# Optimization experiments

Measured on AMD Instinct MI355X. Metric: run time of the kernel, lower is better.

## Reference

```python
import jax, jax.numpy as jnp
import numpy as np

N_DRUG = 20000
N_DIS = 40000
E = 500000
D_IN = 128
D_OUT = 128
SLOPE = 0.01  # F.leaky_relu default negative_slope


def setup_inputs() -> dict:
    key = jax.random.key(0)
    ks = jax.random.split(key, 17)
    s = 1.0 / np.sqrt(D_IN)
    inp = {
        'feat_drug': jax.random.normal(ks[0], (N_DRUG, D_IN), jnp.float32),
        'feat_disease': jax.random.normal(ks[1], (N_DIS, D_IN), jnp.float32),
        'src_ind': jax.random.randint(ks[2], (E,), 0, N_DRUG, jnp.int32),
        'dst_ind': jax.random.randint(ks[3], (E,), 0, N_DIS, jnp.int32),
        'src_rev': jax.random.randint(ks[4], (E,), 0, N_DIS, jnp.int32),
        'dst_rev': jax.random.randint(ks[5], (E,), 0, N_DRUG, jnp.int32),
        'src_dd': jax.random.randint(ks[6], (E,), 0, N_DIS, jnp.int32),
        'dst_dd': jax.random.randint(ks[7], (E,), 0, N_DIS, jnp.int32),
        'W_ind': jax.random.normal(ks[8], (D_IN, D_OUT), jnp.float32) * s,
        'b_ind': jax.random.normal(ks[9], (D_OUT,), jnp.float32) * s,
        'W_rev': jax.random.normal(ks[10], (D_IN, D_OUT), jnp.float32) * s,
        'b_rev': jax.random.normal(ks[11], (D_OUT,), jnp.float32) * s,
        'W_dd': jax.random.normal(ks[12], (D_IN, D_OUT), jnp.float32) * s,
        'b_dd': jax.random.normal(ks[13], (D_OUT,), jnp.float32) * s,
        'a_ind': jax.random.normal(ks[14], (2 * D_OUT,), jnp.float32) * s,
        'a_rev': jax.random.normal(ks[15], (2 * D_OUT,), jnp.float32) * s,
        'a_dd': jax.random.normal(ks[16], (2 * D_OUT,), jnp.float32) * s,
    }
    return inp


def _leaky(x):
    return jnp.where(x >= 0, x, SLOPE * x)


def _etype_softmax_agg(wh_src, wh_dst, src, dst, a, n_dst):
    # per-edge message gather
    m = wh_src[src]                      # [E, D_OUT]
    wd = wh_dst[dst]                     # [E, D_OUT]
    # attn_fc(concat(m, wd)) == m @ a[:D] + wd @ a[D:]
    e = _leaky(m @ a[:D_OUT] + wd @ a[D_OUT:])   # [E]
    # segment softmax over dst (per-node mailbox softmax)
    emax = jax.ops.segment_max(e, dst, num_segments=n_dst)
    ex = jnp.exp(e - emax[dst])
    denom = jax.ops.segment_sum(ex, dst, num_segments=n_dst)
    alpha = ex / denom[dst]
    # weighted scatter-sum aggregation
    return jax.ops.segment_sum(alpha[:, None] * m, dst, num_segments=n_dst)


def reference(feat_drug, feat_disease, src_ind, dst_ind, src_rev, dst_rev,
              src_dd, dst_dd, W_ind, b_ind, W_rev, b_rev, W_dd, b_dd,
              a_ind, a_rev, a_dd):
    # per-etype linear projections of the source node type
    Wh_ind = feat_drug @ W_ind + b_ind       # drug nodes, etype 'indication'
    Wh_rev = feat_disease @ W_rev + b_rev    # disease nodes, etype 'rev_indication'
    Wh_dd = feat_disease @ W_dd + b_dd       # disease nodes, etype 'dd' (self type)
    # indication: drug->disease pairs with dst key Wh_rev_indication
    h_dis = _etype_softmax_agg(Wh_ind, Wh_rev, src_ind, dst_ind, a_ind, N_DIS)
    # dd: same src/dst type, uses Wh_dd on both sides; cross-etype 'sum' reducer
    h_dis = h_dis + _etype_softmax_agg(Wh_dd, Wh_dd, src_dd, dst_dd, a_dd, N_DIS)
    # rev_indication: disease->drug pairs with dst key Wh_indication
    h_drug = _etype_softmax_agg(Wh_rev, Wh_ind, src_rev, dst_rev, a_rev, N_DRUG)
    return (h_drug, h_dis)
```

## Files before the change

### kernel.cpp

```cpp
#include <hip/hip_runtime.h>
#include <hip/hip_bf16.h>

#define N_DRUG 20000
#define N_DIS  40000
#define NE     500000
#define D      128
#define PITCH  136
#define NTOT   100000
#define NQ     (NE / 4)
#define NQ3    (3 * NQ)
#define CSTR   16
#define WSZ    (128 * PITCH)

typedef __hip_bfloat16 bf16;
typedef __attribute__((ext_vector_type(8))) short short8;
typedef __attribute__((ext_vector_type(4))) float floatx4;
typedef __attribute__((ext_vector_type(4))) unsigned short ushortx4;

__device__ __forceinline__ float b2f(bf16 x) { return __bfloat162float(x); }

#define GB_DRUG 313
#define GB_DIS  625
#define GB_ALL  (GB_DRUG + 2 * GB_DIS)
#define GH      ((NQ3 + 255) / 256)

__global__ void k_prep(const float* __restrict__ W_ind, const float* __restrict__ W_rev,
                       const float* __restrict__ W_dd, bf16* __restrict__ WbfT)
{
    const int et = blockIdx.x >> 4;
    const int sl = blockIdx.x & 15;
    const float* W = (et == 0) ? W_ind : (et == 1) ? W_rev : W_dd;
    bf16* out = WbfT + (size_t)et * WSZ;
    int idx = sl * 1024 + threadIdx.x;
#pragma unroll
    for (int r = 0; r < 4; ++r, idx += 256) {
        int k = idx >> 7, n = idx & 127;
        out[n * PITCH + k] = __float2bfloat16(W[idx]);
    }
}

__global__ void k_gh(const float* __restrict__ feat_drug, const float* __restrict__ feat_dis,
                     const bf16* __restrict__ WbfT,
                     const float* __restrict__ b_ind, const float* __restrict__ b_rev,
                     const float* __restrict__ b_dd,
                     const float* __restrict__ a_ind, const float* __restrict__ a_rev,
                     const float* __restrict__ a_dd,
                     bf16* __restrict__ Wh_ind, bf16* __restrict__ Wh_rev,
                     bf16* __restrict__ Wh_dd,
                     float* __restrict__ s_src_ind, float* __restrict__ s_dst_rev,
                     float* __restrict__ s_src_rev, float* __restrict__ s_dst_ind,
                     float* __restrict__ s_src_dd,  float* __restrict__ s_dst_dd,
                     const int4* __restrict__ d_ind, const int4* __restrict__ d_dd,
                     const int4* __restrict__ d_rev, int* __restrict__ cnt,
                     unsigned short* __restrict__ rank)
{
    __shared__ __align__(16) bf16 WT[128 * PITCH];
    __shared__ __align__(16) bf16 FS[64 * PITCH];
    const int tid = threadIdx.x;
    const int blk = blockIdx.x;

    int gemm_blk;
    if (blk < 2 * GH) {
        if (blk & 1) {
            const int i = (blk >> 1) * 256 + tid;
            if (i >= NQ3) return;
            int4 d; int boff;
            if (i < NQ)          { d = d_ind[i];          boff = 0; }
            else if (i < 2 * NQ) { d = d_dd[i - NQ];      boff = 40000; }
            else                 { d = d_rev[i - 2 * NQ]; boff = 80000; }
            ushortx4 r;
            r[0] = (unsigned short)atomicAdd(&cnt[(boff + d.x) * CSTR], 1);
            r[1] = (unsigned short)atomicAdd(&cnt[(boff + d.y) * CSTR], 1);
            r[2] = (unsigned short)atomicAdd(&cnt[(boff + d.z) * CSTR], 1);
            r[3] = (unsigned short)atomicAdd(&cnt[(boff + d.w) * CSTR], 1);
            *(ushortx4*)(rank + 4 * (size_t)i) = r;
            return;
        }
        gemm_blk = blk >> 1;
    } else {
        gemm_blk = GH + (blk - 2 * GH);
    }

    const float *feat, *bias, *a1, *a2;
    const bf16* Wt;
    bf16* Wh; float *s1, *s2;
    int M, row0;
    if (gemm_blk < GB_DRUG) {
        feat = feat_drug; M = N_DRUG; row0 = gemm_blk * 64;
        Wt = WbfT; bias = b_ind; a1 = a_ind; a2 = a_rev + D;
        Wh = Wh_ind; s1 = s_src_ind; s2 = s_dst_rev;
    } else if (gemm_blk < GB_DRUG + GB_DIS) {
        feat = feat_dis; M = N_DIS; row0 = (gemm_blk - GB_DRUG) * 64;
        Wt = WbfT + WSZ; bias = b_rev; a1 = a_rev; a2 = a_ind + D;
        Wh = Wh_rev; s1 = s_src_rev; s2 = s_dst_ind;
    } else {
        feat = feat_dis; M = N_DIS; row0 = (gemm_blk - GB_DRUG - GB_DIS) * 64;
        Wt = WbfT + 2 * WSZ; bias = b_dd; a1 = a_dd; a2 = a_dd + D;
        Wh = Wh_dd; s1 = s_src_dd; s2 = s_dst_dd;
    }

#pragma unroll
    for (int rep = 0; rep < 9; ++rep) {
        int off = rep * 2048 + tid * 8;
        if (off < WSZ)
            *(short8*)(WT + off) = *(const short8*)(Wt + off);
    }
#pragma unroll
    for (int rep = 0; rep < 8; ++rep) {
        int idx = rep * 1024 + tid * 4;
        int r = idx >> 7, k = idx & 127;
        int gr = row0 + r;
        float4 f4 = (gr < M) ? *(const float4*)(feat + (size_t)gr * D + k)
                             : make_float4(0.f, 0.f, 0.f, 0.f);
        FS[r * PITCH + k + 0] = __float2bfloat16(f4.x);
        FS[r * PITCH + k + 1] = __float2bfloat16(f4.y);
        FS[r * PITCH + k + 2] = __float2bfloat16(f4.z);
        FS[r * PITCH + k + 3] = __float2bfloat16(f4.w);
    }
    __syncthreads();

    const int wave = tid >> 6;
    const int lane = tid & 63;
    const int m0   = wave * 16;
    const int arow = lane & 15;
    const int kq   = lane >> 4;

    floatx4 acc[8];
#pragma unroll
    for (int t = 0; t < 8; ++t) acc[t] = (floatx4){0.f, 0.f, 0.f, 0.f};

#pragma unroll
    for (int ks = 0; ks < 4; ++ks) {
        const int kb = ks * 32 + kq * 8;
        short8 afrag = *(const short8*)(FS + (m0 + arow) * PITCH + kb);
#pragma unroll
        for (int t = 0; t < 8; ++t) {
            short8 bfrag = *(const short8*)(WT + (t * 16 + arow) * PITCH + kb);
            acc[t] = __builtin_amdgcn_mfma_f32_16x16x32_bf16(afrag, bfrag, acc[t], 0, 0, 0);
        }
    }

    const int crow = m0 + kq * 4;
    float p1[4] = {0.f, 0.f, 0.f, 0.f};
    float p2[4] = {0.f, 0.f, 0.f, 0.f};
#pragma unroll
    for (int t = 0; t < 8; ++t) {
        const int n = t * 16 + arow;
        const float bn = bias[n], a1n = a1[n], a2n = a2[n];
#pragma unroll
        for (int r = 0; r < 4; ++r) {
            float v = acc[t][r] + bn;
            int gr = row0 + crow + r;
            if (gr < M) Wh[(size_t)gr * D + n] = __float2bfloat16(v);
            p1[r] += v * a1n;
            p2[r] += v * a2n;
        }
    }
#pragma unroll
    for (int r = 0; r < 4; ++r) {
#pragma unroll
        for (int off = 1; off < 16; off <<= 1) {
            p1[r] += __shfl_xor(p1[r], off);
            p2[r] += __shfl_xor(p2[r], off);
        }
    }
    if (arow == 0) {
#pragma unroll
        for (int r = 0; r < 4; ++r) {
            int gr = row0 + crow + r;
            if (gr < M) { s1[gr] = p1[r]; s2[gr] = p2[r]; }
        }
    }
}

__global__ void k_base(const int* __restrict__ cnt, int* __restrict__ base,
                       int* __restrict__ cntp, int* __restrict__ total, int n)
{
    __shared__ int sd[256];
    __shared__ int sbase;
    const int tid = threadIdx.x;
    const int gid = blockIdx.x * 256 + tid;
    int c = (gid < n) ? cnt[gid * CSTR] : 0;
    sd[tid] = c;
    __syncthreads();
    for (int off = 1; off < 256; off <<= 1) {
        int v = (tid >= off) ? sd[tid - off] : 0;
        __syncthreads();
        sd[tid] += v;
        __syncthreads();
    }
    if (tid == 255) sbase = atomicAdd(total, sd[255]);
    __syncthreads();
    if (gid < n) {
        base[gid] = sbase + sd[tid] - c;
        cntp[gid] = c;
    }
}

__global__ void k_fill_rank(const int4* __restrict__ s_ind, const int4* __restrict__ d_ind,
                            const int4* __restrict__ s_dd,  const int4* __restrict__ d_dd,
                            const int4* __restrict__ s_rev, const int4* __restrict__ d_rev,
                            const int* __restrict__ base, const unsigned short* __restrict__ rank,
                            unsigned short* __restrict__ col)
{
    const int i = blockIdx.x * 256 + threadIdx.x;
    if (i >= NQ3) return;
    int4 d, s; int boff;
    if (i < NQ)          { d = d_ind[i];              s = s_ind[i];          boff = 0; }
    else if (i < 2 * NQ) { int j = i - NQ;     d = d_dd[j];  s = s_dd[j];  boff = 40000; }
    else                 { int j = i - 2 * NQ; d = d_rev[j]; s = s_rev[j]; boff = 80000; }
    ushortx4 r = *(const ushortx4*)(rank + 4 * (size_t)i);
    col[base[boff + d.x] + r[0]] = (unsigned short)s.x;
    col[base[boff + d.y] + r[1]] = (unsigned short)s.y;
    col[base[boff + d.z] + r[2]] = (unsigned short)s.z;
    col[base[boff + d.w] + r[3]] = (unsigned short)s.w;
}

__device__ __forceinline__ float2 agg_seg(int b, int c, const unsigned short* __restrict__ col,
                                          const float* __restrict__ ssrc, float sdv,
                                          const bf16* __restrict__ Whs, int lane)
{
    float ax = 0.f, ay = 0.f, dpart = 0.f;
    for (int t0 = 0; t0 < c; t0 += 64) {
        const int rem = c - t0;
        const int k = rem < 64 ? rem : 64;
        int myc = 0; float myex = 0.f;
        if (lane < k) {
            myc = col[b + t0 + lane];
            float e = ssrc[myc] + sdv;
            e = (e >= 0.f) ? e : 0.01f * e;
            myex = __expf(fminf(e, 30.f));
        }
        dpart += myex;
        const int kk = (k + 7) & ~7;
        for (int j = 0; j < kk; j += 8) {
            int sv[8]; float ev[8]; __hip_bfloat162 w[8];
#pragma unroll
            for (int u = 0; u < 8; ++u) {
                sv[u] = __shfl(myc, j + u);
                ev[u] = __shfl(myex, j + u);
            }
#pragma unroll
            for (int u = 0; u < 8; ++u)
                w[u] = *(const __hip_bfloat162*)(Whs + (size_t)sv[u] * D + 2 * lane);
#pragma unroll
            for (int u = 0; u < 8; ++u) {
                ax += ev[u] * b2f(w[u].x);
                ay += ev[u] * b2f(w[u].y);
            }
        }
    }
    float denom = dpart;
#pragma unroll
    for (int off = 32; off; off >>= 1) denom += __shfl_xor(denom, off);
    const float inv = (c > 0) ? 1.f / denom : 0.f;
    return make_float2(ax * inv, ay * inv);
}

__global__ void k_agg(const int* __restrict__ base, const int* __restrict__ cnt,
                      const unsigned short* __restrict__ col,
                      const float* __restrict__ ss_ind, const float* __restrict__ sd_ind,
                      const bf16* __restrict__ Wh_ind,
                      const float* __restrict__ ss_dd, const float* __restrict__ sd_dd,
                      const bf16* __restrict__ Wh_dd,
                      const float* __restrict__ ss_rev, const float* __restrict__ sd_rev,
                      const bf16* __restrict__ Wh_rev,
                      float* __restrict__ out_dis, float* __restrict__ out_drug)
{
    const int g    = (int)((blockIdx.x * blockDim.x + threadIdx.x) >> 6);
    const int lane = threadIdx.x & 63;
    if (g < N_DIS) {
        float2 r1 = agg_seg(base[g], cnt[g], col, ss_ind, sd_ind[g], Wh_ind, lane);
        float2 r2 = agg_seg(base[40000 + g], cnt[40000 + g], col, ss_dd, sd_dd[g], Wh_dd, lane);
        *(float2*)(out_dis + (size_t)g * D + 2 * lane) = make_float2(r1.x + r2.x, r1.y + r2.y);
    } else if (g < N_DIS + N_DRUG) {
        const int gg = g - N_DIS;
        float2 r = agg_seg(base[80000 + gg], cnt[80000 + gg], col, ss_rev, sd_rev[gg], Wh_rev, lane);
        *(float2*)(out_drug + (size_t)gg * D + 2 * lane) = r;
    }
}

extern "C" void kernel_launch(void* const* d_in, const int* in_sizes, int n_in,
                              void* d_out, int out_size, void* d_ws, size_t ws_size,
                              hipStream_t stream)
{
    const float* feat_drug = (const float*)d_in[0];
    const float* feat_dis  = (const float*)d_in[1];
    const int*   src_ind   = (const int*)d_in[2];
    const int*   dst_ind   = (const int*)d_in[3];
    const int*   src_rev   = (const int*)d_in[4];
    const int*   dst_rev   = (const int*)d_in[5];
    const int*   src_dd    = (const int*)d_in[6];
    const int*   dst_dd    = (const int*)d_in[7];
    const float* W_ind     = (const float*)d_in[8];
    const float* b_ind     = (const float*)d_in[9];
    const float* W_rev     = (const float*)d_in[10];
    const float* b_rev     = (const float*)d_in[11];
    const float* W_dd      = (const float*)d_in[12];
    const float* b_dd      = (const float*)d_in[13];
    const float* a_ind     = (const float*)d_in[14];
    const float* a_rev     = (const float*)d_in[15];
    const float* a_dd      = (const float*)d_in[16];

    float* out_drug = (float*)d_out;
    float* out_dis  = (float*)d_out + (size_t)N_DRUG * D;

    char* ws = (char*)d_ws;
    size_t off = 0;
    auto alloc = [&](size_t bytes) -> void* {
        void* p = ws + off;
        off += (bytes + 255) & ~(size_t)255;
        return p;
    };

    bf16* Wh_ind = (bf16*)alloc(sizeof(bf16) * (size_t)N_DRUG * D);
    bf16* Wh_rev = (bf16*)alloc(sizeof(bf16) * (size_t)N_DIS * D);
    bf16* Wh_dd  = (bf16*)alloc(sizeof(bf16) * (size_t)N_DIS * D);
    bf16* WbfT   = (bf16*)alloc(sizeof(bf16) * 3 * WSZ);

    float* s_src_ind = (float*)alloc(sizeof(float) * N_DRUG);
    float* s_dst_rev = (float*)alloc(sizeof(float) * N_DRUG);
    float* s_src_rev = (float*)alloc(sizeof(float) * N_DIS);
    float* s_dst_ind = (float*)alloc(sizeof(float) * N_DIS);
    float* s_src_dd  = (float*)alloc(sizeof(float) * N_DIS);
    float* s_dst_dd  = (float*)alloc(sizeof(float) * N_DIS);

    unsigned short* col  = (unsigned short*)alloc(sizeof(unsigned short) * 3 * NE);
    unsigned short* rank = (unsigned short*)alloc(sizeof(unsigned short) * 3 * NE);
    int* base = (int*)alloc(sizeof(int) * NTOT);
    int* cntp = (int*)alloc(sizeof(int) * NTOT);

    const size_t nzero = (size_t)NTOT * CSTR + 4;
    int* zr  = (int*)alloc(sizeof(int) * nzero);
    int* cnt = zr;
    int* total = zr + (size_t)NTOT * CSTR;

    hipMemsetAsync(zr, 0, sizeof(int) * nzero, stream);

    k_prep<<<48, 256, 0, stream>>>(W_ind, W_rev, W_dd, WbfT);

    k_gh<<<GB_ALL + GH, 256, 0, stream>>>(
        feat_drug, feat_dis, WbfT, b_ind, b_rev, b_dd,
        a_ind, a_rev, a_dd, Wh_ind, Wh_rev, Wh_dd,
        s_src_ind, s_dst_rev, s_src_rev, s_dst_ind, s_src_dd, s_dst_dd,
        (const int4*)dst_ind, (const int4*)dst_dd, (const int4*)dst_rev, cnt, rank);

    k_base<<<(NTOT + 255) / 256, 256, 0, stream>>>(cnt, base, cntp, total, NTOT);
    k_fill_rank<<<GH, 256, 0, stream>>>((const int4*)src_ind, (const int4*)dst_ind,
                                        (const int4*)src_dd, (const int4*)dst_dd,
                                        (const int4*)src_rev, (const int4*)dst_rev,
                                        base, rank, col);

    k_agg<<<(N_DIS + N_DRUG + 3) / 4, 256, 0, stream>>>(base, cntp, col,
                                                        s_src_ind, s_dst_ind, Wh_ind,
                                                        s_src_dd, s_dst_dd, Wh_dd,
                                                        s_src_rev, s_dst_rev, Wh_rev,
                                                        out_dis, out_drug);
}
```

Measured before the change: 251.1 us.

## Split disease aggregation across two waves and fuse memset into weight prep

Each disease node's two edge-type aggregations (indication and dd) now run on separate wavefronts, and the partial results are combined through shared memory. Before, one wave processed both segments one after the other. This raises parallelism and shortens the per-wave critical path, at the cost of a block barrier and more blocks. The hipMemsetAsync of the counter buffer is also folded into the weight-transpose kernel as extra zeroing blocks, removing one launch.

```diff
diff --git a/kernel.cpp b/kernel.cpp
--- a/kernel.cpp
+++ b/kernel.cpp
@@ -23,19 +23,28 @@
 #define GB_DIS  625
 #define GB_ALL  (GB_DRUG + 2 * GB_DIS)
 #define GH      ((NQ3 + 255) / 256)
-
-__global__ void k_prep(const float* __restrict__ W_ind, const float* __restrict__ W_rev,
-                       const float* __restrict__ W_dd, bf16* __restrict__ WbfT)
-{
-    const int et = blockIdx.x >> 4;
-    const int sl = blockIdx.x & 15;
-    const float* W = (et == 0) ? W_ind : (et == 1) ? W_rev : W_dd;
-    bf16* out = WbfT + (size_t)et * WSZ;
-    int idx = sl * 1024 + threadIdx.x;
-#pragma unroll
-    for (int r = 0; r < 4; ++r, idx += 256) {
-        int k = idx >> 7, n = idx & 127;
-        out[n * PITCH + k] = __float2bfloat16(W[idx]);
+#define NZERO4  ((NTOT * CSTR + 4) / 4)
+
+__global__ void k_init(const float* __restrict__ W_ind, const float* __restrict__ W_rev,
+                       const float* __restrict__ W_dd, bf16* __restrict__ WbfT,
+                       int4* __restrict__ zr4)
+{
+    const int blk = blockIdx.x;
+    if (blk < 48) {
+        const int et = blk >> 4;
+        const int sl = blk & 15;
+        const float* W = (et == 0) ? W_ind : (et == 1) ? W_rev : W_dd;
+        bf16* out = WbfT + (size_t)et * WSZ;
+        int idx = sl * 1024 + threadIdx.x;
+#pragma unroll
+        for (int r = 0; r < 4; ++r, idx += 256) {
+            int k = idx >> 7, n = idx & 127;
+            out[n * PITCH + k] = __float2bfloat16(W[idx]);
+        }
+    } else {
+        const int4 z = make_int4(0, 0, 0, 0);
+        for (int j = (blk - 48) * 256 + threadIdx.x; j < NZERO4; j += 400 * 256)
+            zr4[j] = z;
     }
 }
 
@@ -257,6 +266,8 @@
     return make_float2(ax * inv, ay * inv);
 }
 
+#define AGG_DIS_BLK (N_DIS / 2)
+#define AGG_BLKS    (AGG_DIS_BLK + N_DRUG / 4)
 __global__ void k_agg(const int* __restrict__ base, const int* __restrict__ cnt,
                       const unsigned short* __restrict__ col,
                       const float* __restrict__ ss_ind, const float* __restrict__ sd_ind,
@@ -267,16 +278,30 @@
                       const bf16* __restrict__ Wh_rev,
                       float* __restrict__ out_dis, float* __restrict__ out_drug)
 {
-    const int g    = (int)((blockIdx.x * blockDim.x + threadIdx.x) >> 6);
+    __shared__ float2 part[4][64];
+    const int blk  = blockIdx.x;
+    const int wave = threadIdx.x >> 6;
     const int lane = threadIdx.x & 63;
-    if (g < N_DIS) {
-        float2 r1 = agg_seg(base[g], cnt[g], col, ss_ind, sd_ind[g], Wh_ind, lane);
-        float2 r2 = agg_seg(base[40000 + g], cnt[40000 + g], col, ss_dd, sd_dd[g], Wh_dd, lane);
-        *(float2*)(out_dis + (size_t)g * D + 2 * lane) = make_float2(r1.x + r2.x, r1.y + r2.y);
-    } else if (g < N_DIS + N_DRUG) {
-        const int gg = g - N_DIS;
-        float2 r = agg_seg(base[80000 + gg], cnt[80000 + gg], col, ss_rev, sd_rev[gg], Wh_rev, lane);
-        *(float2*)(out_drug + (size_t)gg * D + 2 * lane) = r;
+    if (blk < AGG_DIS_BLK) {
+        const int node = blk * 2 + (wave >> 1);
+        float2 r;
+        if ((wave & 1) == 0)
+            r = agg_seg(base[node], cnt[node], col, ss_ind, sd_ind[node], Wh_ind, lane);
+        else
+            r = agg_seg(base[40000 + node], cnt[40000 + node], col, ss_dd, sd_dd[node], Wh_dd, lane);
+        part[wave][lane] = r;
+        __syncthreads();
+        if ((wave & 1) == 0) {
+            float2 o = part[wave + 1][lane];
+            *(float2*)(out_dis + (size_t)node * D + 2 * lane) =
+                make_float2(r.x + o.x, r.y + o.y);
+        }
+    } else {
+        const int gg = (blk - AGG_DIS_BLK) * 4 + wave;
+        if (gg < N_DRUG) {
+            float2 r = agg_seg(base[80000 + gg], cnt[80000 + gg], col, ss_rev, sd_rev[gg], Wh_rev, lane);
+            *(float2*)(out_drug + (size_t)gg * D + 2 * lane) = r;
+        }
     }
 }
 
@@ -335,9 +360,7 @@
     int* cnt = zr;
     int* total = zr + (size_t)NTOT * CSTR;
 
-    hipMemsetAsync(zr, 0, sizeof(int) * nzero, stream);
-
-    k_prep<<<48, 256, 0, stream>>>(W_ind, W_rev, W_dd, WbfT);
+    k_init<<<448, 256, 0, stream>>>(W_ind, W_rev, W_dd, WbfT, (int4*)zr);
 
     k_gh<<<GB_ALL + GH, 256, 0, stream>>>(
         feat_drug, feat_dis, WbfT, b_ind, b_rev, b_dd,
@@ -351,9 +374,9 @@
                                         (const int4*)src_rev, (const int4*)dst_rev,
                                         base, rank, col);
 
-    k_agg<<<(N_DIS + N_DRUG + 3) / 4, 256, 0, stream>>>(base, cntp, col,
-                                                        s_src_ind, s_dst_ind, Wh_ind,
-                                                        s_src_dd, s_dst_dd, Wh_dd,
-                                                        s_src_rev, s_dst_rev, Wh_rev,
-                                                        out_dis, out_drug);
-}
+    k_agg<<<AGG_BLKS, 256, 0, stream>>>(base, cntp, col,
+                                        s_src_ind, s_dst_ind, Wh_ind,
+                                        s_src_dd, s_dst_dd, Wh_dd,
+                                        s_src_rev, s_dst_rev, Wh_rev,
+                                        out_dis, out_drug);
+}
```

Measured after the change: 255.1 us. No clear change (+1.6%).
